# Kernel tuning notes

Hardware: AMD Instinct MI355X
Metric: run time of the kernel (lower is better)

## Reference

```python
import jax, jax.numpy as jnp
import numpy as np

B, T, D_MODEL, D_HEAD = 4, 2048, 1024, 64

def setup_inputs() -> dict:
    key = jax.random.key(0)
    k1, k2, k3, k4 = jax.random.split(key, 4)
    x = jax.random.normal(k1, (B, T, D_MODEL), dtype=jnp.float32)
    # Linear(d_model, d_head) weights stored as [d_model, d_head] for x @ W
    s = 1.0 / np.sqrt(D_MODEL)
    W_Q = jax.random.normal(k2, (D_MODEL, D_HEAD), dtype=jnp.float32) * s
    W_K = jax.random.normal(k3, (D_MODEL, D_HEAD), dtype=jnp.float32) * s
    W_V = jax.random.normal(k4, (D_MODEL, D_HEAD), dtype=jnp.float32) * s
    return {"x": x, "W_Q": W_Q, "W_K": W_K, "W_V": W_V}

def reference(x, W_Q, W_K, W_V):
    d_head = W_Q.shape[-1]
    Q = jnp.einsum('btm,md->btd', x, W_Q)
    K = jnp.einsum('btm,md->btd', x, W_K)
    V = jnp.einsum('btm,md->btd', x, W_V)
    A = jnp.einsum('bid,bjd->bij', Q, K) / jnp.sqrt(jnp.asarray(d_head, x.dtype))
    T_ = x.shape[1]
    causal = jnp.tril(jnp.ones((T_, T_), dtype=bool))  # [T, T]
    A = jnp.where(causal, A, -jnp.inf)
    A = jax.nn.softmax(A, axis=-1)
    return jnp.einsum('bij,bjd->bid', A, V)
```

## Files before the change

kernel.cpp:

```cpp
#include <hip/hip_runtime.h>
#include <hip/hip_bf16.h>

#define NB 4
#define NT 2048
#define DM 1024
#define DH 64
#define CHUNK3 3
#define SLOTS 6

typedef __attribute__((ext_vector_type(8))) short bf16x8;
typedef __attribute__((ext_vector_type(4))) float f32x4;
typedef unsigned short u16;
typedef unsigned int u32;

static __device__ __forceinline__ u16 f2b(float f) {
    __hip_bfloat16 h = __float2bfloat16(f);
    return __builtin_bit_cast(u16, h);
}
static __device__ __forceinline__ float b2f(u16 h) {
    return __builtin_bit_cast(float, (u32)h << 16);
}
static __device__ __forceinline__ void gld16(const void* g, void* l) {
    __builtin_amdgcn_global_load_lds((const __attribute__((address_space(1))) void*)g,
                                     (__attribute__((address_space(3))) void*)l, 16, 0, 0);
}
#define BAR() __builtin_amdgcn_s_barrier()
#define SBAR() __builtin_amdgcn_sched_barrier(0)

__global__ __launch_bounds__(256) void wt_conv(
    const float* __restrict__ WQ, const float* __restrict__ WK,
    const float* __restrict__ WV, u16* __restrict__ wt)
{
    __shared__ u16 tl[64][68];
    const int which = blockIdx.y, kt = blockIdx.x;
    const float* W = (which == 0) ? WQ : (which == 1) ? WK : WV;
    #pragma unroll
    for (int i = 0; i < 4; ++i) {
        int r = (threadIdx.x >> 4) + i * 16;
        int c = (threadIdx.x & 15) * 4;
        float4 v = *(const float4*)&W[(size_t)(kt * 64 + r) * DH + c];
        tl[r][c] = f2b(v.x); tl[r][c + 1] = f2b(v.y);
        tl[r][c + 2] = f2b(v.z); tl[r][c + 3] = f2b(v.w);
    }
    __syncthreads();
    int d = threadIdx.x >> 2, kc = (threadIdx.x & 3) * 16;
    u16 buf[16];
    #pragma unroll
    for (int j = 0; j < 16; ++j) buf[j] = tl[kc + j][d];
    u16* dst = wt + which * 65536 + d * 1024 + kt * 64 + kc;
    *(uint4*)dst = *(uint4*)&buf[0];
    *(uint4*)(dst + 8) = *(uint4*)&buf[8];
}

__global__ __launch_bounds__(256) void qkv_gemm(
    const float* __restrict__ x, const u16* __restrict__ wt,
    u16* __restrict__ Qb, u16* __restrict__ Kb, u16* __restrict__ Vt)
{
    __shared__ u16 xbuf[2][4096];
    __shared__ u16 wsm[2][4096];
    const int tid = threadIdx.x, lane = tid & 63, w = tid >> 6;
    const int l15 = lane & 15, g = lane >> 4;
    const int row0 = blockIdx.x * 64;
    const int which = blockIdx.y;
    const u16* Wg = wt + which * 65536;

    const int xr_ = tid >> 2, xc4 = tid & 3;
    const float* xsrc = x + (size_t)(row0 + xr_) * DM + xc4 * 16;
    const u32 xsw = (u32)((xr_ & 7) << 4);
    const u32 xa0 = (u32)(xr_ * 128 + xc4 * 32) ^ xsw;
    const u32 xa1 = (u32)(xr_ * 128 + xc4 * 32 + 16) ^ xsw;

    f32x4 xv[4];
    auto xload = [&](int kt) {
        const float* p = xsrc + kt * 64;
        xv[0] = *(const f32x4*)(p);
        xv[1] = *(const f32x4*)(p + 4);
        xv[2] = *(const f32x4*)(p + 8);
        xv[3] = *(const f32x4*)(p + 12);
    };
    auto stageW = [&](int kt, int bi) {
        #pragma unroll
        for (int i = 0; i < 2; ++i) {
            u32 D = (u32)(w * 2048 + i * 1024 + lane * 16);
            u32 r = D >> 7, c = D & 127;
            u32 cs = c ^ ((r & 7) << 4);
            gld16(Wg + (size_t)r * 1024 + kt * 64 + (cs >> 1),
                  (char*)&wsm[bi][0] + w * 2048 + i * 1024);
        }
    };

    f32x4 acc[4];
    #pragma unroll
    for (int i = 0; i < 4; ++i) acc[i] = {0.f, 0.f, 0.f, 0.f};

    xload(0);
    stageW(0, 0);
    const int arow = w * 16 + l15;
    const u32 asw = (u32)((arow & 7) << 4);

    #pragma unroll
    for (int kt = 0; kt < 16; ++kt) {
        const int cur = kt & 1;
        asm volatile("s_waitcnt vmcnt(2)" ::: "memory");
        {
            u16 tmp[16];
            #pragma unroll
            for (int i = 0; i < 4; ++i)
                #pragma unroll
                for (int j = 0; j < 4; ++j) tmp[i * 4 + j] = f2b(xv[i][j]);
            *(uint4*)((char*)&xbuf[cur][0] + xa0) = *(uint4*)&tmp[0];
            *(uint4*)((char*)&xbuf[cur][0] + xa1) = *(uint4*)&tmp[8];
        }
        if (kt < 15) {
            xload(kt + 1);
            stageW(kt + 1, cur ^ 1);
            asm volatile("s_waitcnt vmcnt(6)" ::: "memory");
        } else {
            asm volatile("s_waitcnt vmcnt(0)" ::: "memory");
        }
        asm volatile("s_waitcnt lgkmcnt(0)" ::: "memory");
        BAR();
        SBAR();
        const char* xb = (const char*)&xbuf[cur][0];
        const char* wb = (const char*)&wsm[cur][0];
        #pragma unroll
        for (int ks = 0; ks < 2; ++ks) {
            bf16x8 afrag = *(const bf16x8*)(xb + ((u32)(arow * 128 + ks * 64 + g * 16) ^ asw));
            __builtin_amdgcn_s_setprio(1);
            #pragma unroll
            for (int nt = 0; nt < 4; ++nt) {
                int brow = nt * 16 + l15;
                u32 bb = (u32)(brow * 128 + ks * 64 + g * 16);
                bf16x8 bfrag = *(const bf16x8*)(wb + (bb ^ ((brow & 7) << 4)));
                acc[nt] = __builtin_amdgcn_mfma_f32_16x16x32_bf16(afrag, bfrag, acc[nt], 0, 0, 0);
            }
            __builtin_amdgcn_s_setprio(0);
        }
        BAR();
    }
    #pragma unroll
    for (int nt = 0; nt < 4; ++nt) {
        int dcol = nt * 16 + l15;
        #pragma unroll
        for (int r = 0; r < 4; ++r) {
            int row = row0 + w * 16 + g * 4 + r;
            float v = acc[nt][r];
            if (which == 0)      Qb[(size_t)row * DH + dcol] = f2b(v * 0.125f);
            else if (which == 1) Kb[(size_t)row * DH + dcol] = f2b(v);
            else { int bb2 = row >> 11, t = row & 2047;
                   Vt[(size_t)bb2 * DH * NT + (size_t)dcol * NT + t] = f2b(v); }
        }
    }
}

__global__ __launch_bounds__(256) void attn(
    const u16* __restrict__ Qb, const u16* __restrict__ Kb,
    const u16* __restrict__ Vt, u16* __restrict__ pOt, float* __restrict__ pml)
{
    __shared__ u16 k_lds[2][8192];
    __shared__ u16 v_lds[2][8192];
    __shared__ f32x4 p_lds[4][256];

    const int tid = threadIdx.x, lane = tid & 63, w = tid >> 6;
    const int l15 = lane & 15, g = lane >> 4;
    const int b = blockIdx.y;

    int flat = blockIdx.x, qb = 0, nc, nt128;
    for (;;) {
        nt128 = (qb + 2) >> 1;
        nc = (nt128 + CHUNK3 - 1) / CHUNK3;
        if (flat < nc) break;
        flat -= nc; ++qb;
    }
    const int chunk = flat;
    const int t0 = chunk * CHUNK3;
    const int t1 = min(t0 + CHUNK3, nt128);
    const int tD = nt128 - 1;
    const int delta = qb * 64 - tD * 128;
    const int q0 = qb * 64;

    const u16* Qg = Qb + ((size_t)b * NT + q0 + w * 16) * DH;
    const u16* Kg = Kb + (size_t)b * NT * DH;
    const u16* Vg = Vt + (size_t)b * DH * NT;

    auto stage = [&](int t, int bi) {
        const int j0 = t * 128;
        #pragma unroll
        for (int i = 0; i < 4; ++i) {
            u32 D = (u32)(w * 4096 + i * 1024 + lane * 16);
            {
                u32 r = D >> 7, c = D & 127;
                u32 cs = c ^ ((r & 7) << 4);
                gld16(Kg + (size_t)(j0 + r) * DH + (cs >> 1),
                      (char*)&k_lds[bi][0] + w * 4096 + i * 1024);
            }
            {
                u32 r = D >> 8, c = D & 255;
                u32 cs = c ^ ((r & 15) << 4);
                gld16(Vg + (size_t)r * NT + j0 + (cs >> 1),
                      (char*)&v_lds[bi][0] + w * 4096 + i * 1024);
            }
        }
    };
    stage(t0, 0);

    bf16x8 qf[2];
    qf[0] = *(const bf16x8*)(Qg + l15 * DH + g * 8);
    qf[1] = *(const bf16x8*)(Qg + l15 * DH + 32 + g * 8);

    float m_run = -INFINITY, l_run = 0.f;
    f32x4 oacc[4];
    #pragma unroll
    for (int nt = 0; nt < 4; ++nt) oacc[nt] = {0.f, 0.f, 0.f, 0.f};

    char* pw = (char*)&p_lds[w][0];
    const u32 pswz = (u32)((l15 & 15) << 4);
    const int q_local = w * 16 + l15;

    for (int t = t0; t < t1; ++t) {
        const int cur = (t - t0) & 1;
        if (t + 1 < t1) {
            stage(t + 1, cur ^ 1);
            asm volatile("s_waitcnt vmcnt(8)" ::: "memory");
        } else {
            asm volatile("s_waitcnt vmcnt(0)" ::: "memory");
        }
        BAR();
        SBAR();
        const char* kb = (const char*)&k_lds[cur][0];
        const char* vb = (const char*)&v_lds[cur][0];

        f32x4 sacc[8];
        #pragma unroll
        for (int f = 0; f < 8; ++f) sacc[f] = {0.f, 0.f, 0.f, 0.f};
        __builtin_amdgcn_s_setprio(1);
        #pragma unroll
        for (int ks = 0; ks < 2; ++ks) {
            #pragma unroll
            for (int f = 0; f < 8; ++f) {
                int arow = f * 16 + l15;
                u32 aa = (u32)(arow * 128 + ks * 64 + g * 16);
                bf16x8 kf = *(const bf16x8*)(kb + (aa ^ ((arow & 7) << 4)));
                sacc[f] = __builtin_amdgcn_mfma_f32_16x16x32_bf16(kf, qf[ks], sacc[f], 0, 0, 0);
            }
        }
        __builtin_amdgcn_s_setprio(0);
        if (t == tD) {
            #pragma unroll
            for (int f = 0; f < 8; ++f)
                #pragma unroll
                for (int r = 0; r < 4; ++r)
                    if (f * 16 + g * 4 + r > delta + q_local) sacc[f][r] = -1e30f;
        }
        float mx = -INFINITY;
        #pragma unroll
        for (int f = 0; f < 8; ++f) {
            float a = fmaxf(fmaxf(sacc[f][0], sacc[f][1]),
                            fmaxf(sacc[f][2], sacc[f][3]));
            mx = fmaxf(mx, a);
        }
        mx = fmaxf(mx, __shfl_xor(mx, 16));
        mx = fmaxf(mx, __shfl_xor(mx, 32));
        const float m_new = fmaxf(m_run, mx);
        const float alpha = __expf(m_run - m_new);
        float p[8][4];
        float ps = 0.f;
        #pragma unroll
        for (int f = 0; f < 8; ++f)
            #pragma unroll
            for (int r = 0; r < 4; ++r) {
                float pv = __expf(sacc[f][r] - m_new);
                p[f][r] = pv; ps += pv;
            }
        ps += __shfl_xor(ps, 16);
        ps += __shfl_xor(ps, 32);
        l_run = l_run * alpha + ps;
        m_run = m_new;
        #pragma unroll
        for (int nt = 0; nt < 4; ++nt)
            #pragma unroll
            for (int r = 0; r < 4; ++r) oacc[nt][r] *= alpha;

        #pragma unroll
        for (int f = 0; f < 8; ++f) {
            uint2 pk;
            pk.x = (u32)f2b(p[f][0]) | ((u32)f2b(p[f][1]) << 16);
            pk.y = (u32)f2b(p[f][2]) | ((u32)f2b(p[f][3]) << 16);
            u32 a = (u32)(l15 * 256 + f * 32 + g * 8) ^ pswz;
            *(uint2*)(pw + a) = pk;
        }
        bf16x8 pb_[4];
        #pragma unroll
        for (int ksj = 0; ksj < 4; ++ksj)
            pb_[ksj] = *(const bf16x8*)(pw + ((u32)(l15 * 256 + ksj * 64 + g * 16) ^ pswz));

        __builtin_amdgcn_s_setprio(1);
        #pragma unroll
        for (int ksj = 0; ksj < 4; ++ksj) {
            #pragma unroll
            for (int nt = 0; nt < 4; ++nt) {
                int arow = nt * 16 + l15;
                u32 aa = (u32)(arow * 256 + ksj * 64 + g * 16);
                bf16x8 vf = *(const bf16x8*)(vb + (aa ^ ((arow & 15) << 4)));
                oacc[nt] = __builtin_amdgcn_mfma_f32_16x16x32_bf16(vf, pb_[ksj], oacc[nt], 0, 0, 0);
            }
        }
        __builtin_amdgcn_s_setprio(0);
        BAR();
    }

    const int slot = (b * 32 + qb) * SLOTS + chunk;
    u16* Op = pOt + (size_t)slot * 4096;
    #pragma unroll
    for (int nt = 0; nt < 4; ++nt)
        #pragma unroll
        for (int r = 0; r < 4; ++r)
            Op[(nt * 16 + g * 4 + r) * 64 + w * 16 + l15] = f2b(oacc[nt][r]);
    if (g == 0) {
        float* mlp = pml + (size_t)slot * 128;
        mlp[(w * 16 + l15) * 2]     = m_run;
        mlp[(w * 16 + l15) * 2 + 1] = l_run;
    }
}

__global__ __launch_bounds__(256) void merge(
    const u16* __restrict__ pOt, const float* __restrict__ pml,
    float* __restrict__ out)
{
    __shared__ float tl[64][65];
    const int bq = blockIdx.x;
    const int b = bq >> 5, qb = bq & 31;
    const int nt128 = (qb + 2) >> 1;
    const int nc = (nt128 + CHUNK3 - 1) / CHUNK3;
    const int base = bq * SLOTS;
    const int q = threadIdx.x & 63, ds = threadIdx.x >> 6;

    float m = -INFINITY;
    for (int c = 0; c < nc; ++c)
        m = fmaxf(m, pml[(size_t)(base + c) * 128 + q * 2]);
    float lsum = 0.f;
    float acc[16];
    #pragma unroll
    for (int i = 0; i < 16; ++i) acc[i] = 0.f;
    for (int c = 0; c < nc; ++c) {
        const float mc = pml[(size_t)(base + c) * 128 + q * 2];
        const float lc = pml[(size_t)(base + c) * 128 + q * 2 + 1];
        const float wc = __expf(mc - m);
        lsum += wc * lc;
        const u16* Op = pOt + (size_t)(base + c) * 4096;
        #pragma unroll
        for (int i = 0; i < 16; ++i)
            acc[i] += wc * b2f(Op[(ds * 16 + i) * 64 + q]);
    }
    const float inv = 1.f / lsum;
    #pragma unroll
    for (int i = 0; i < 16; ++i) tl[q][ds * 16 + i] = acc[i] * inv;
    __syncthreads();
    const int q2 = threadIdx.x >> 2, dc = threadIdx.x & 3;
    float* orow = out + ((size_t)b * NT + qb * 64 + q2) * 64 + dc * 16;
    #pragma unroll
    for (int j4 = 0; j4 < 4; ++j4) {
        float4 v = { tl[q2][dc * 16 + j4 * 4 + 0], tl[q2][dc * 16 + j4 * 4 + 1],
                     tl[q2][dc * 16 + j4 * 4 + 2], tl[q2][dc * 16 + j4 * 4 + 3] };
        *(float4*)&orow[j4 * 4] = v;
    }
}

extern "C" void kernel_launch(void* const* d_in, const int* in_sizes, int n_in,
                              void* d_out, int out_size, void* d_ws, size_t ws_size,
                              hipStream_t stream) {
    const float* x  = (const float*)d_in[0];
    const float* WQ = (const float*)d_in[1];
    const float* WK = (const float*)d_in[2];
    const float* WV = (const float*)d_in[3];
    float* out = (float*)d_out;

    char* ws = (char*)d_ws;
    u16*   Qb  = (u16*)ws;
    u16*   Kb  = (u16*)(ws + 1048576);
    u16*   Vt  = (u16*)(ws + 2097152);
    u16*   Wt  = (u16*)(ws + 3145728);
    u16*   pOt = (u16*)(ws + 3538944);
    float* pml = (float*)(ws + 3538944 + 6291456);

    wt_conv<<<dim3(16, 3), 256, 0, stream>>>(WQ, WK, WV, Wt);
    qkv_gemm<<<dim3(128, 3), 256, 0, stream>>>(x, Wt, Qb, Kb, Vt);
    attn<<<dim3(102, NB), 256, 0, stream>>>(Qb, Kb, Vt, pOt, pml);
    merge<<<NB * 32, 256, 0, stream>>>(pOt, pml, out);
}
```

Before: 42.79 us.

## Deepen QKV GEMM prefetch pipeline to two stages and drop trailing barrier

Raises the QKV projection GEMM's prefetch distance from one to two K-tiles. x registers are double-buffered and the W tiles in LDS become a 4-slot ring, so the end-of-iteration barrier can be removed. The aim is to hide more global-load latency and cut one barrier per iteration. In exchange it uses more registers and LDS, which may lower occupancy, and the waitcnt accounting is delicate: the xbuf write could race with the previous iteration's reads now that the trailing barrier is gone.

```diff
diff --git a/kernel.cpp b/kernel.cpp
--- a/kernel.cpp
+++ b/kernel.cpp
@@ -57,7 +57,7 @@
     u16* __restrict__ Qb, u16* __restrict__ Kb, u16* __restrict__ Vt)
 {
     __shared__ u16 xbuf[2][4096];
-    __shared__ u16 wsm[2][4096];
+    __shared__ u16 wsm[4][4096];
     const int tid = threadIdx.x, lane = tid & 63, w = tid >> 6;
     const int l15 = lane & 15, g = lane >> 4;
     const int row0 = blockIdx.x * 64;
@@ -70,13 +70,13 @@
     const u32 xa0 = (u32)(xr_ * 128 + xc4 * 32) ^ xsw;
     const u32 xa1 = (u32)(xr_ * 128 + xc4 * 32 + 16) ^ xsw;
 
-    f32x4 xv[4];
-    auto xload = [&](int kt) {
+    f32x4 xv[2][4];
+    auto xload = [&](int kt, int s) {
         const float* p = xsrc + kt * 64;
-        xv[0] = *(const f32x4*)(p);
-        xv[1] = *(const f32x4*)(p + 4);
-        xv[2] = *(const f32x4*)(p + 8);
-        xv[3] = *(const f32x4*)(p + 12);
+        xv[s][0] = *(const f32x4*)(p);
+        xv[s][1] = *(const f32x4*)(p + 4);
+        xv[s][2] = *(const f32x4*)(p + 8);
+        xv[s][3] = *(const f32x4*)(p + 12);
     };
     auto stageW = [&](int kt, int bi) {
         #pragma unroll
@@ -93,36 +93,41 @@
     #pragma unroll
     for (int i = 0; i < 4; ++i) acc[i] = {0.f, 0.f, 0.f, 0.f};
 
-    xload(0);
+    xload(0, 0);
     stageW(0, 0);
+    xload(1, 1);
+    stageW(1, 1);
+
     const int arow = w * 16 + l15;
     const u32 asw = (u32)((arow & 7) << 4);
 
     #pragma unroll
     for (int kt = 0; kt < 16; ++kt) {
-        const int cur = kt & 1;
-        asm volatile("s_waitcnt vmcnt(2)" ::: "memory");
+        const int xs_ = kt & 1;
+        const int wslot = kt & 3;
+        if (kt < 15)      asm volatile("s_waitcnt vmcnt(8)" ::: "memory");
+        else              asm volatile("s_waitcnt vmcnt(2)" ::: "memory");
         {
             u16 tmp[16];
             #pragma unroll
             for (int i = 0; i < 4; ++i)
                 #pragma unroll
-                for (int j = 0; j < 4; ++j) tmp[i * 4 + j] = f2b(xv[i][j]);
-            *(uint4*)((char*)&xbuf[cur][0] + xa0) = *(uint4*)&tmp[0];
-            *(uint4*)((char*)&xbuf[cur][0] + xa1) = *(uint4*)&tmp[8];
-        }
-        if (kt < 15) {
-            xload(kt + 1);
-            stageW(kt + 1, cur ^ 1);
-            asm volatile("s_waitcnt vmcnt(6)" ::: "memory");
-        } else {
-            asm volatile("s_waitcnt vmcnt(0)" ::: "memory");
-        }
+                for (int j = 0; j < 4; ++j) tmp[i * 4 + j] = f2b(xv[xs_][i][j]);
+            *(uint4*)((char*)&xbuf[xs_][0] + xa0) = *(uint4*)&tmp[0];
+            *(uint4*)((char*)&xbuf[xs_][0] + xa1) = *(uint4*)&tmp[8];
+        }
+        if (kt + 2 < 16) {
+            xload(kt + 2, xs_);
+            stageW(kt + 2, (kt + 2) & 3);
+        }
+        if (kt < 14)      asm volatile("s_waitcnt vmcnt(12)" ::: "memory");
+        else if (kt == 14) asm volatile("s_waitcnt vmcnt(6)" ::: "memory");
+        else              asm volatile("s_waitcnt vmcnt(0)" ::: "memory");
         asm volatile("s_waitcnt lgkmcnt(0)" ::: "memory");
         BAR();
         SBAR();
-        const char* xb = (const char*)&xbuf[cur][0];
-        const char* wb = (const char*)&wsm[cur][0];
+        const char* xb = (const char*)&xbuf[xs_][0];
+        const char* wb = (const char*)&wsm[wslot][0];
         #pragma unroll
         for (int ks = 0; ks < 2; ++ks) {
             bf16x8 afrag = *(const bf16x8*)(xb + ((u32)(arow * 128 + ks * 64 + g * 16) ^ asw));
@@ -136,7 +141,6 @@
             }
             __builtin_amdgcn_s_setprio(0);
         }
-        BAR();
     }
     #pragma unroll
     for (int nt = 0; nt < 4; ++nt) {
```

Result: faster. 41.16 us (-3.8%).
